# Kernel optimization log

Hardware: AMD Instinct MI355X
Metric: run time of the kernel (lower is better)

## Reference

```python
import jax, jax.numpy as jnp
import numpy as np

B, DIM_IN, T = 16, 512, 2048
DIM_OUT2 = 512 * 2  # dim_out * 2 (GLU halves it)
K = 3
STYLE = 128
SCALE_CONV = 1.0 / np.sqrt(DIM_IN * K ** 2).astype(np.float32)  # fan_in = dim_in * k^2 (as in source)
SCALE_LIN = 1.0 / np.sqrt(STYLE).astype(np.float32)


def setup_inputs() -> dict:
    key = jax.random.key(0)
    ks = jax.random.split(key, 6)
    x = jax.random.normal(ks[0], (B, DIM_IN, T), dtype=jnp.float32)
    c_src = jax.random.normal(ks[1], (B, STYLE), dtype=jnp.float32)
    c_trg = jax.random.normal(ks[2], (B, STYLE), dtype=jnp.float32)
    # EqualLinear params (lr_mul=1): weight ~ N(0,1), bias filled with bias_init=1
    w_s = jax.random.normal(ks[3], (DIM_IN, STYLE), dtype=jnp.float32)
    b_s = jnp.ones((DIM_IN,), dtype=jnp.float32)
    w_b = jax.random.normal(ks[4], (DIM_IN, STYLE), dtype=jnp.float32)
    b_b = jnp.ones((DIM_IN,), dtype=jnp.float32)
    weight = jax.random.normal(ks[5], (1, DIM_OUT2, DIM_IN, K), dtype=jnp.float32)
    return {"x": x, "c_src": c_src, "c_trg": c_trg,
            "w_s": w_s, "b_s": b_s, "w_b": w_b, "b_b": b_b, "weight": weight}


def reference(x, c_src, c_trg, w_s, b_s, w_b, b_b, weight):
    bsz, cin, t = x.shape
    cout = weight.shape[1]  # dim_out * 2
    k = weight.shape[3]
    # EqualLinear: F.linear(c, w*scale, bias)
    s = (c_trg @ (w_s * SCALE_LIN).T + b_s).reshape(bsz, 1, cin, 1)
    beta = (c_trg @ (w_b * SCALE_LIN).T + b_b).reshape(bsz, 1, cin, 1)
    w = SCALE_CONV * (weight * s + beta)               # [B, Cout, Cin, K]
    demod = jax.lax.rsqrt(jnp.sum(w * w, axis=(2, 3)) + 1e-8)   # [B, Cout]
    demod_mean = jnp.mean(w.reshape(bsz, cout, -1), axis=2)      # [B, Cout]
    w = (w - demod_mean[:, :, None, None]) * demod[:, :, None, None]
    # batch-as-groups conv1d
    w = w.reshape(bsz * cout, cin, k)
    xr = x.reshape(1, bsz * cin, t)
    out = jax.lax.conv_general_dilated(
        xr, w, window_strides=(1,), padding=[(k // 2, k // 2)],
        dimension_numbers=("NCH", "OIH", "NCH"), feature_group_count=bsz)
    out = out.reshape(bsz, cout, -1)
    a, g = jnp.split(out, 2, axis=1)  # GLU on channel dim
    return a * jax.nn.sigmoid(g)
```

## Files before the change

### kernel.cpp

```cpp
#include <hip/hip_runtime.h>
#include <math.h>

typedef __attribute__((ext_vector_type(8))) short short8;
typedef __attribute__((ext_vector_type(4))) float f32x4;
typedef unsigned short ushortT;

#define NB     16
#define CIN    512
#define TT     2048
#define COUT2  1024
#define NSTYLE 128
#define KKTOT  1536
#define TPAD   2050
#define NKT    24

#define SCALE_LIN  0.088388347648318447f
#define SCALE_CONV 0.014731391274719736f

__device__ __forceinline__ ushortT f2bf(float f) {
  union { float f; unsigned u; } v; v.f = f;
  unsigned r = v.u + 0x7fffu + ((v.u >> 16) & 1u);
  return (ushortT)(r >> 16);
}

__device__ __forceinline__ void gload16(const void* g, void* l) {
  __builtin_amdgcn_global_load_lds(
      (const __attribute__((address_space(1))) void*)g,
      (__attribute__((address_space(3))) void*)l, 16, 0, 0);
}

__global__ void style_kernel(const float* __restrict__ c_trg,
                             const float* __restrict__ w_s, const float* __restrict__ b_s,
                             const float* __restrict__ w_b, const float* __restrict__ b_b,
                             float* __restrict__ s, float* __restrict__ beta,
                             ushortT* __restrict__ xT) {
  int gid = blockIdx.x * 256 + threadIdx.x;
  int b = gid >> 9, ci = gid & 511;
  const float* ct = c_trg + b * NSTYLE;
  const float* ws = w_s + ci * NSTYLE;
  const float* wb = w_b + ci * NSTYLE;
  float as = 0.f, ab = 0.f;
#pragma unroll 8
  for (int j = 0; j < NSTYLE; ++j) {
    float c = ct[j];
    as += c * ws[j];
    ab += c * wb[j];
  }
  s[gid]    = as * SCALE_LIN + b_s[ci];
  beta[gid] = ab * SCALE_LIN + b_b[ci];
  xT[(size_t)b * TPAD * CIN + ci] = 0;
  xT[((size_t)b * TPAD + TPAD - 1) * CIN + ci] = 0;
}

__global__ void xpose_kernel(const float* __restrict__ x, ushortT* __restrict__ xT) {
  int b = blockIdx.z, ct = blockIdx.y, tt = blockIdx.x;
  int t0 = tt * 64, ci0 = ct * 64;
  __shared__ float tile[64][65];
  const float* xB = x + (size_t)b * CIN * TT;
  int rr = threadIdx.x >> 4;
  int c4 = threadIdx.x & 15;
#pragma unroll
  for (int it = 0; it < 4; ++it) {
    int ci = rr + it * 16;
    float4 v = *(const float4*)(xB + (size_t)(ci0 + ci) * TT + t0 + c4 * 4);
    tile[ci][c4 * 4 + 0] = v.x; tile[ci][c4 * 4 + 1] = v.y;
    tile[ci][c4 * 4 + 2] = v.z; tile[ci][c4 * 4 + 3] = v.w;
  }
  __syncthreads();
  ushortT* xTB = xT + (size_t)b * TPAD * CIN;
#pragma unroll
  for (int it = 0; it < 4; ++it) {
    int t = rr + it * 16;
    ushort4 o;
    o.x = f2bf(tile[c4 * 4 + 0][t]); o.y = f2bf(tile[c4 * 4 + 1][t]);
    o.z = f2bf(tile[c4 * 4 + 2][t]); o.w = f2bf(tile[c4 * 4 + 3][t]);
    *(ushort4*)(xTB + (size_t)(1 + t0 + t) * CIN + ci0 + c4 * 4) = o;
  }
}

__global__ void modw_kernel(const float* __restrict__ weight,
                            const float* __restrict__ s, const float* __restrict__ beta,
                            ushortT* __restrict__ wnorm) {
  int co = blockIdx.x, b = blockIdx.y, tid = threadIdx.x;
  int ci = tid * 2;
  const float* wp = weight + (size_t)co * CIN * 3 + (size_t)ci * 3;
  float s0 = s[b * CIN + ci],     s1 = s[b * CIN + ci + 1];
  float e0 = beta[b * CIN + ci],  e1 = beta[b * CIN + ci + 1];
  float w0 = SCALE_CONV * (wp[0] * s0 + e0);
  float w1 = SCALE_CONV * (wp[1] * s0 + e0);
  float w2 = SCALE_CONV * (wp[2] * s0 + e0);
  float w3 = SCALE_CONV * (wp[3] * s1 + e1);
  float w4 = SCALE_CONV * (wp[4] * s1 + e1);
  float w5 = SCALE_CONV * (wp[5] * s1 + e1);
  float sum = w0 + w1 + w2 + w3 + w4 + w5;
  float sq  = w0*w0 + w1*w1 + w2*w2 + w3*w3 + w4*w4 + w5*w5;
#pragma unroll
  for (int off = 32; off; off >>= 1) {
    sum += __shfl_xor(sum, off);
    sq  += __shfl_xor(sq,  off);
  }
  __shared__ float rs[4], rq[4];
  if ((tid & 63) == 0) { rs[tid >> 6] = sum; rq[tid >> 6] = sq; }
  __syncthreads();
  float tsum = rs[0] + rs[1] + rs[2] + rs[3];
  float tsq  = rq[0] + rq[1] + rq[2] + rq[3];
  float mean  = tsum * (1.0f / 1536.0f);
  float demod = rsqrtf(tsq + 1e-8f);
  int r = ((co & 511) << 1) | (co >> 9);
  ushortT* dst = wnorm + ((size_t)b * COUT2 + r) * KKTOT;
  ushort2 p0, p1, p2;
  p0.x = f2bf((w0 - mean) * demod); p0.y = f2bf((w3 - mean) * demod);
  p1.x = f2bf((w1 - mean) * demod); p1.y = f2bf((w4 - mean) * demod);
  p2.x = f2bf((w2 - mean) * demod); p2.y = f2bf((w5 - mean) * demod);
  *(ushort2*)(dst +        ci) = p0;
  *(ushort2*)(dst +  512 + ci) = p1;
  *(ushort2*)(dst + 1024 + ci) = p2;
}


#define AFRAG(d, s, f) (*(const short8*)(ldsc + ((d) * 4 + (s)) * 16384 + aoff + (f) * 1024))
#define BFRAG(d, s, g) (*(const short8*)(ldsc + ((d) * 4 + 2 + (s)) * 16384 + boff + (g) * 1024))

#define STAGE_A(d, s, kt) do {                                                   \
    int kc_ = (kt) * 64 + (s) * 32;                                              \
    gload16(wB + (size_t)(co0 + r0) * KKTOT + kc_ + jbs8,                        \
            ldsw + ((d) * 4 + (s)) * 8192 + tid * 8);                            \
    gload16(wB + (size_t)(co0 + r0 + 128) * KKTOT + kc_ + jbs8,                  \
            ldsw + ((d) * 4 + (s)) * 8192 + 4096 + tid * 8);                     \
  } while (0)

#define STAGE_B(d, s, kt) do {                                                   \
    int kc_ = (kt) * 64 + (s) * 32;                                              \
    int tap_ = kc_ >> 9; int ci_ = kc_ & 511;                                    \
    gload16(xB + (size_t)(t0 + r0 + tap_) * CIN + ci_ + jbs8,                    \
            ldsw + ((d) * 4 + 2 + (s)) * 8192 + tid * 8);                        \
    gload16(xB + (size_t)(t0 + r0 + 128 + tap_) * CIN + ci_ + jbs8,              \
            ldsw + ((d) * 4 + 2 + (s)) * 8192 + 4096 + tid * 8);                 \
  } while (0)

#define PHASE(d, s, mh, STAGES, VMN) do {                                        \
    short8 a0 = AFRAG(d, s, (mh) * 4 + 0);                                       \
    short8 a1 = AFRAG(d, s, (mh) * 4 + 1);                                       \
    short8 a2 = AFRAG(d, s, (mh) * 4 + 2);                                       \
    short8 a3 = AFRAG(d, s, (mh) * 4 + 3);                                       \
    if ((mh) == 0) {                                                             \
      bf0 = BFRAG(d, s, 0); bf1 = BFRAG(d, s, 1);                                \
      bf2 = BFRAG(d, s, 2); bf3 = BFRAG(d, s, 3);                                \
    }                                                                            \
    STAGES;                                                                      \
    if ((VMN) == 6)      asm volatile("s_waitcnt vmcnt(6)" ::: "memory");        \
    else if ((VMN) == 0) asm volatile("s_waitcnt vmcnt(0)" ::: "memory");        \
    __builtin_amdgcn_sched_barrier(0);                                           \
    __builtin_amdgcn_s_barrier();                                                \
    __builtin_amdgcn_sched_barrier(0);                                           \
    __builtin_amdgcn_s_setprio(1);                                               \
    acc[(mh)*4+0][0] = __builtin_amdgcn_mfma_f32_16x16x32_bf16(a0, bf0, acc[(mh)*4+0][0], 0, 0, 0); \
    acc[(mh)*4+0][1] = __builtin_amdgcn_mfma_f32_16x16x32_bf16(a0, bf1, acc[(mh)*4+0][1], 0, 0, 0); \
    acc[(mh)*4+0][2] = __builtin_amdgcn_mfma_f32_16x16x32_bf16(a0, bf2, acc[(mh)*4+0][2], 0, 0, 0); \
    acc[(mh)*4+0][3] = __builtin_amdgcn_mfma_f32_16x16x32_bf16(a0, bf3, acc[(mh)*4+0][3], 0, 0, 0); \
    acc[(mh)*4+1][0] = __builtin_amdgcn_mfma_f32_16x16x32_bf16(a1, bf0, acc[(mh)*4+1][0], 0, 0, 0); \
    acc[(mh)*4+1][1] = __builtin_amdgcn_mfma_f32_16x16x32_bf16(a1, bf1, acc[(mh)*4+1][1], 0, 0, 0); \
    acc[(mh)*4+1][2] = __builtin_amdgcn_mfma_f32_16x16x32_bf16(a1, bf2, acc[(mh)*4+1][2], 0, 0, 0); \
    acc[(mh)*4+1][3] = __builtin_amdgcn_mfma_f32_16x16x32_bf16(a1, bf3, acc[(mh)*4+1][3], 0, 0, 0); \
    acc[(mh)*4+2][0] = __builtin_amdgcn_mfma_f32_16x16x32_bf16(a2, bf0, acc[(mh)*4+2][0], 0, 0, 0); \
    acc[(mh)*4+2][1] = __builtin_amdgcn_mfma_f32_16x16x32_bf16(a2, bf1, acc[(mh)*4+2][1], 0, 0, 0); \
    acc[(mh)*4+2][2] = __builtin_amdgcn_mfma_f32_16x16x32_bf16(a2, bf2, acc[(mh)*4+2][2], 0, 0, 0); \
    acc[(mh)*4+2][3] = __builtin_amdgcn_mfma_f32_16x16x32_bf16(a2, bf3, acc[(mh)*4+2][3], 0, 0, 0); \
    acc[(mh)*4+3][0] = __builtin_amdgcn_mfma_f32_16x16x32_bf16(a3, bf0, acc[(mh)*4+3][0], 0, 0, 0); \
    acc[(mh)*4+3][1] = __builtin_amdgcn_mfma_f32_16x16x32_bf16(a3, bf1, acc[(mh)*4+3][1], 0, 0, 0); \
    acc[(mh)*4+3][2] = __builtin_amdgcn_mfma_f32_16x16x32_bf16(a3, bf2, acc[(mh)*4+3][2], 0, 0, 0); \
    acc[(mh)*4+3][3] = __builtin_amdgcn_mfma_f32_16x16x32_bf16(a3, bf3, acc[(mh)*4+3][3], 0, 0, 0); \
    __builtin_amdgcn_s_setprio(0);                                               \
    __builtin_amdgcn_sched_barrier(0);                                           \
    __builtin_amdgcn_s_barrier();                                                \
    __builtin_amdgcn_sched_barrier(0);                                           \
  } while (0)

__global__ __launch_bounds__(512, 2)
void conv_gemm8(const ushortT* __restrict__ wnorm, const ushortT* __restrict__ xT,
                float* __restrict__ out) {
  extern __shared__ ushortT ldsw[];
  const char* ldsc = (const char*)ldsw;

  int orig = blockIdx.x;
  int wgid = (orig & 7) * 64 + (orig >> 3);
  int b  = wgid >> 5;
  int i5 = wgid & 31;
  int mp = i5 >> 4, r2 = i5 & 15;
  int nt = r2 >> 1, mt = mp * 2 + (r2 & 1);
  int co0 = mt * 256, t0 = nt * 256;

  int tid = threadIdx.x;
  int l = tid & 63, w = tid >> 6;
  int wm = w & 1, wn = w >> 1;

  int r0 = tid >> 2;
  int jbs8 = (((tid & 3) ^ ((r0 >> 1) & 3)) << 3);
  int cb = ((l >> 4) ^ ((l >> 1) & 3));
  int aoff = (wm * 128 + (l & 15)) * 64 + cb * 16;
  int boff = (wn * 64  + (l & 15)) * 64 + cb * 16;

  const ushortT* wB = wnorm + (size_t)b * COUT2 * KKTOT;
  const ushortT* xB = xT + (size_t)b * TPAD * CIN;

  f32x4 acc[8][4];
#pragma unroll
  for (int i = 0; i < 8; ++i)
#pragma unroll
    for (int j = 0; j < 4; ++j)
      acc[i][j] = (f32x4){0.f, 0.f, 0.f, 0.f};
  short8 bf0 = {}, bf1 = {}, bf2 = {}, bf3 = {};

  STAGE_A(0, 0, 0); STAGE_B(0, 0, 0); STAGE_A(0, 1, 0); STAGE_B(0, 1, 0);
  STAGE_B(1, 0, 1); STAGE_A(1, 0, 1); STAGE_B(1, 1, 1);
  asm volatile("s_waitcnt vmcnt(6)" ::: "memory");
  __builtin_amdgcn_sched_barrier(0);
  __builtin_amdgcn_s_barrier();
  __builtin_amdgcn_sched_barrier(0);

  for (int j = 0; j < 11; ++j) {
    int kt1 = 2 * j + 1;
    int ktn0 = 2 * j + 2, ktn1 = 2 * j + 3;
    PHASE(0, 0, 0, STAGE_A(1, 1, kt1),  -1);
    PHASE(0, 0, 1, STAGE_B(0, 0, ktn0), -1);
    PHASE(0, 1, 0, STAGE_A(0, 0, ktn0), -1);
    PHASE(0, 1, 1, STAGE_B(0, 1, ktn0),  6);
    PHASE(1, 0, 0, STAGE_A(0, 1, ktn0), -1);
    PHASE(1, 0, 1, STAGE_B(1, 0, ktn1), -1);
    PHASE(1, 1, 0, STAGE_A(1, 0, ktn1), -1);
    PHASE(1, 1, 1, STAGE_B(1, 1, ktn1),  6);
  }
  PHASE(0, 0, 0, STAGE_A(1, 1, 23), -1);
  PHASE(0, 0, 1, {}, -1);
  PHASE(0, 1, 0, {}, -1);
  PHASE(0, 1, 1, {},  0);
  PHASE(1, 0, 0, {}, -1);
  PHASE(1, 0, 1, {}, -1);
  PHASE(1, 1, 0, {}, -1);
  PHASE(1, 1, 1, {}, -1);

#pragma unroll
  for (int f = 0; f < 8; ++f) {
    int cop = co0 + wm * 128 + f * 16 + ((l >> 4) << 2);
    int c = cop >> 1;
    size_t obase = ((size_t)b * (COUT2 / 2) + c) * TT;
#pragma unroll
    for (int g = 0; g < 4; ++g) {
      int t = t0 + wn * 64 + g * 16 + (l & 15);
      f32x4 v = acc[f][g];
      out[obase + t]      = v.x / (1.f + __expf(-v.y));
      out[obase + TT + t] = v.z / (1.f + __expf(-v.w));
    }
  }
}

extern "C" void kernel_launch(void* const* d_in, const int* in_sizes, int n_in,
                              void* d_out, int out_size, void* d_ws, size_t ws_size,
                              hipStream_t stream) {
  const float* x      = (const float*)d_in[0];
  const float* c_trg  = (const float*)d_in[2];
  const float* w_s    = (const float*)d_in[3];
  const float* b_s    = (const float*)d_in[4];
  const float* w_b    = (const float*)d_in[5];
  const float* b_b    = (const float*)d_in[6];
  const float* weight = (const float*)d_in[7];
  float* out = (float*)d_out;

  char* ws = (char*)d_ws;
  float*   s     = (float*)ws;
  float*   beta  = (float*)(ws + 32768);
  ushortT* xT    = (ushortT*)(ws + 65536);
  ushortT* wnorm = (ushortT*)(ws + 65536 + 33587200);

  hipFuncSetAttribute((const void*)conv_gemm8,
                      hipFuncAttributeMaxDynamicSharedMemorySize, 131072);

  style_kernel<<<32, 256, 0, stream>>>(c_trg, w_s, b_s, w_b, b_b, s, beta, xT);
  xpose_kernel<<<dim3(32, 8, 16), 256, 0, stream>>>(x, xT);
  modw_kernel<<<dim3(1024, 16), 256, 0, stream>>>(weight, s, beta, wnorm);
  conv_gemm8<<<512, 512, 131072, stream>>>(wnorm, xT, out);
}
```

Baseline: 136.8 us.

## Double-buffer LDS fragment registers to prefetch next phase during MFMA

Restructures the GEMM main loop so each phase issues LDS reads for the next phase's A/B fragments into alternate register sets before its MFMA block, overlapping LDS latency with matrix math. The vmcnt waits move to the end of phases with adjusted counts. This doubles fragment register usage (32 short8 vectors), which risks spills or occupancy pressure under launch_bounds(512,2), and it changes the correctness-critical sync ordering between global loads and LDS reads.

Result: no change. 136.4 us (-0.3%).

```diff
diff --git a/kernel.cpp b/kernel.cpp
--- a/kernel.cpp
+++ b/kernel.cpp
@@ -121,6 +121,20 @@
 #define AFRAG(d, s, f) (*(const short8*)(ldsc + ((d) * 4 + (s)) * 16384 + aoff + (f) * 1024))
 #define BFRAG(d, s, g) (*(const short8*)(ldsc + ((d) * 4 + 2 + (s)) * 16384 + boff + (g) * 1024))
 
+#define RDA(as_, d, s, mh) do {              \
+    as_##0 = AFRAG(d, s, (mh) * 4 + 0);      \
+    as_##1 = AFRAG(d, s, (mh) * 4 + 1);      \
+    as_##2 = AFRAG(d, s, (mh) * 4 + 2);      \
+    as_##3 = AFRAG(d, s, (mh) * 4 + 3);      \
+  } while (0)
+
+#define RDB(bs_, d, s) do {                  \
+    bs_##0 = BFRAG(d, s, 0);                 \
+    bs_##1 = BFRAG(d, s, 1);                 \
+    bs_##2 = BFRAG(d, s, 2);                 \
+    bs_##3 = BFRAG(d, s, 3);                 \
+  } while (0)
+
 #define STAGE_A(d, s, kt) do {                                                   \
     int kc_ = (kt) * 64 + (s) * 32;                                              \
     gload16(wB + (size_t)(co0 + r0) * KKTOT + kc_ + jbs8,                        \
@@ -138,40 +152,33 @@
             ldsw + ((d) * 4 + 2 + (s)) * 8192 + 4096 + tid * 8);                 \
   } while (0)
 
-#define PHASE(d, s, mh, STAGES, VMN) do {                                        \
-    short8 a0 = AFRAG(d, s, (mh) * 4 + 0);                                       \
-    short8 a1 = AFRAG(d, s, (mh) * 4 + 1);                                       \
-    short8 a2 = AFRAG(d, s, (mh) * 4 + 2);                                       \
-    short8 a3 = AFRAG(d, s, (mh) * 4 + 3);                                       \
-    if ((mh) == 0) {                                                             \
-      bf0 = BFRAG(d, s, 0); bf1 = BFRAG(d, s, 1);                                \
-      bf2 = BFRAG(d, s, 2); bf3 = BFRAG(d, s, 3);                                \
-    }                                                                            \
+#define PHASE(mh, au_, bu_, RD_CODE, STAGES, ENDVM) do {                         \
+    RD_CODE;                                                                     \
     STAGES;                                                                      \
-    if ((VMN) == 6)      asm volatile("s_waitcnt vmcnt(6)" ::: "memory");        \
-    else if ((VMN) == 0) asm volatile("s_waitcnt vmcnt(0)" ::: "memory");        \
     __builtin_amdgcn_sched_barrier(0);                                           \
     __builtin_amdgcn_s_barrier();                                                \
     __builtin_amdgcn_sched_barrier(0);                                           \
     __builtin_amdgcn_s_setprio(1);                                               \
-    acc[(mh)*4+0][0] = __builtin_amdgcn_mfma_f32_16x16x32_bf16(a0, bf0, acc[(mh)*4+0][0], 0, 0, 0); \
-    acc[(mh)*4+0][1] = __builtin_amdgcn_mfma_f32_16x16x32_bf16(a0, bf1, acc[(mh)*4+0][1], 0, 0, 0); \
-    acc[(mh)*4+0][2] = __builtin_amdgcn_mfma_f32_16x16x32_bf16(a0, bf2, acc[(mh)*4+0][2], 0, 0, 0); \
-    acc[(mh)*4+0][3] = __builtin_amdgcn_mfma_f32_16x16x32_bf16(a0, bf3, acc[(mh)*4+0][3], 0, 0, 0); \
-    acc[(mh)*4+1][0] = __builtin_amdgcn_mfma_f32_16x16x32_bf16(a1, bf0, acc[(mh)*4+1][0], 0, 0, 0); \
-    acc[(mh)*4+1][1] = __builtin_amdgcn_mfma_f32_16x16x32_bf16(a1, bf1, acc[(mh)*4+1][1], 0, 0, 0); \
-    acc[(mh)*4+1][2] = __builtin_amdgcn_mfma_f32_16x16x32_bf16(a1, bf2, acc[(mh)*4+1][2], 0, 0, 0); \
-    acc[(mh)*4+1][3] = __builtin_amdgcn_mfma_f32_16x16x32_bf16(a1, bf3, acc[(mh)*4+1][3], 0, 0, 0); \
-    acc[(mh)*4+2][0] = __builtin_amdgcn_mfma_f32_16x16x32_bf16(a2, bf0, acc[(mh)*4+2][0], 0, 0, 0); \
-    acc[(mh)*4+2][1] = __builtin_amdgcn_mfma_f32_16x16x32_bf16(a2, bf1, acc[(mh)*4+2][1], 0, 0, 0); \
-    acc[(mh)*4+2][2] = __builtin_amdgcn_mfma_f32_16x16x32_bf16(a2, bf2, acc[(mh)*4+2][2], 0, 0, 0); \
-    acc[(mh)*4+2][3] = __builtin_amdgcn_mfma_f32_16x16x32_bf16(a2, bf3, acc[(mh)*4+2][3], 0, 0, 0); \
-    acc[(mh)*4+3][0] = __builtin_amdgcn_mfma_f32_16x16x32_bf16(a3, bf0, acc[(mh)*4+3][0], 0, 0, 0); \
-    acc[(mh)*4+3][1] = __builtin_amdgcn_mfma_f32_16x16x32_bf16(a3, bf1, acc[(mh)*4+3][1], 0, 0, 0); \
-    acc[(mh)*4+3][2] = __builtin_amdgcn_mfma_f32_16x16x32_bf16(a3, bf2, acc[(mh)*4+3][2], 0, 0, 0); \
-    acc[(mh)*4+3][3] = __builtin_amdgcn_mfma_f32_16x16x32_bf16(a3, bf3, acc[(mh)*4+3][3], 0, 0, 0); \
+    acc[(mh)*4+0][0] = __builtin_amdgcn_mfma_f32_16x16x32_bf16(au_##0, bu_##0, acc[(mh)*4+0][0], 0, 0, 0); \
+    acc[(mh)*4+0][1] = __builtin_amdgcn_mfma_f32_16x16x32_bf16(au_##0, bu_##1, acc[(mh)*4+0][1], 0, 0, 0); \
+    acc[(mh)*4+0][2] = __builtin_amdgcn_mfma_f32_16x16x32_bf16(au_##0, bu_##2, acc[(mh)*4+0][2], 0, 0, 0); \
+    acc[(mh)*4+0][3] = __builtin_amdgcn_mfma_f32_16x16x32_bf16(au_##0, bu_##3, acc[(mh)*4+0][3], 0, 0, 0); \
+    acc[(mh)*4+1][0] = __builtin_amdgcn_mfma_f32_16x16x32_bf16(au_##1, bu_##0, acc[(mh)*4+1][0], 0, 0, 0); \
+    acc[(mh)*4+1][1] = __builtin_amdgcn_mfma_f32_16x16x32_bf16(au_##1, bu_##1, acc[(mh)*4+1][1], 0, 0, 0); \
+    acc[(mh)*4+1][2] = __builtin_amdgcn_mfma_f32_16x16x32_bf16(au_##1, bu_##2, acc[(mh)*4+1][2], 0, 0, 0); \
+    acc[(mh)*4+1][3] = __builtin_amdgcn_mfma_f32_16x16x32_bf16(au_##1, bu_##3, acc[(mh)*4+1][3], 0, 0, 0); \
+    acc[(mh)*4+2][0] = __builtin_amdgcn_mfma_f32_16x16x32_bf16(au_##2, bu_##0, acc[(mh)*4+2][0], 0, 0, 0); \
+    acc[(mh)*4+2][1] = __builtin_amdgcn_mfma_f32_16x16x32_bf16(au_##2, bu_##1, acc[(mh)*4+2][1], 0, 0, 0); \
+    acc[(mh)*4+2][2] = __builtin_amdgcn_mfma_f32_16x16x32_bf16(au_##2, bu_##2, acc[(mh)*4+2][2], 0, 0, 0); \
+    acc[(mh)*4+2][3] = __builtin_amdgcn_mfma_f32_16x16x32_bf16(au_##2, bu_##3, acc[(mh)*4+2][3], 0, 0, 0); \
+    acc[(mh)*4+3][0] = __builtin_amdgcn_mfma_f32_16x16x32_bf16(au_##3, bu_##0, acc[(mh)*4+3][0], 0, 0, 0); \
+    acc[(mh)*4+3][1] = __builtin_amdgcn_mfma_f32_16x16x32_bf16(au_##3, bu_##1, acc[(mh)*4+3][1], 0, 0, 0); \
+    acc[(mh)*4+3][2] = __builtin_amdgcn_mfma_f32_16x16x32_bf16(au_##3, bu_##2, acc[(mh)*4+3][2], 0, 0, 0); \
+    acc[(mh)*4+3][3] = __builtin_amdgcn_mfma_f32_16x16x32_bf16(au_##3, bu_##3, acc[(mh)*4+3][3], 0, 0, 0); \
     __builtin_amdgcn_s_setprio(0);                                               \
     __builtin_amdgcn_sched_barrier(0);                                           \
+    if ((ENDVM) == 8)      asm volatile("s_waitcnt vmcnt(8)" ::: "memory");      \
+    else if ((ENDVM) == 0) asm volatile("s_waitcnt vmcnt(0)" ::: "memory");      \
     __builtin_amdgcn_s_barrier();                                                \
     __builtin_amdgcn_sched_barrier(0);                                           \
   } while (0)
@@ -209,7 +216,10 @@
 #pragma unroll
     for (int j = 0; j < 4; ++j)
       acc[i][j] = (f32x4){0.f, 0.f, 0.f, 0.f};
-  short8 bf0 = {}, bf1 = {}, bf2 = {}, bf3 = {};
+  short8 ax0 = {}, ax1 = {}, ax2 = {}, ax3 = {};
+  short8 ay0 = {}, ay1 = {}, ay2 = {}, ay3 = {};
+  short8 bx0 = {}, bx1 = {}, bx2 = {}, bx3 = {};
+  short8 by0 = {}, by1 = {}, by2 = {}, by3 = {};
 
   STAGE_A(0, 0, 0); STAGE_B(0, 0, 0); STAGE_A(0, 1, 0); STAGE_B(0, 1, 0);
   STAGE_B(1, 0, 1); STAGE_A(1, 0, 1); STAGE_B(1, 1, 1);
@@ -217,27 +227,29 @@
   __builtin_amdgcn_sched_barrier(0);
   __builtin_amdgcn_s_barrier();
   __builtin_amdgcn_sched_barrier(0);
+  RDA(ax, 0, 0, 0);
+  RDB(bx, 0, 0);
 
   for (int j = 0; j < 11; ++j) {
     int kt1 = 2 * j + 1;
     int ktn0 = 2 * j + 2, ktn1 = 2 * j + 3;
-    PHASE(0, 0, 0, STAGE_A(1, 1, kt1),  -1);
-    PHASE(0, 0, 1, STAGE_B(0, 0, ktn0), -1);
-    PHASE(0, 1, 0, STAGE_A(0, 0, ktn0), -1);
-    PHASE(0, 1, 1, STAGE_B(0, 1, ktn0),  6);
-    PHASE(1, 0, 0, STAGE_A(0, 1, ktn0), -1);
-    PHASE(1, 0, 1, STAGE_B(1, 0, ktn1), -1);
-    PHASE(1, 1, 0, STAGE_A(1, 0, ktn1), -1);
-    PHASE(1, 1, 1, STAGE_B(1, 1, ktn1),  6);
-  }
-  PHASE(0, 0, 0, STAGE_A(1, 1, 23), -1);
-  PHASE(0, 0, 1, {}, -1);
-  PHASE(0, 1, 0, {}, -1);
-  PHASE(0, 1, 1, {},  0);
-  PHASE(1, 0, 0, {}, -1);
-  PHASE(1, 0, 1, {}, -1);
-  PHASE(1, 1, 0, {}, -1);
-  PHASE(1, 1, 1, {}, -1);
+    PHASE(0, ax, bx, { RDA(ay, 0, 0, 1); },                  STAGE_A(1, 1, kt1),   8);
+    PHASE(1, ay, bx, { RDA(ax, 0, 1, 0); RDB(by, 0, 1); },   STAGE_B(0, 0, ktn0), -1);
+    PHASE(0, ax, by, { RDA(ay, 0, 1, 1); },                  STAGE_A(0, 0, ktn0),  8);
+    PHASE(1, ay, by, { RDA(ax, 1, 0, 0); RDB(bx, 1, 0); },   STAGE_B(0, 1, ktn0), -1);
+    PHASE(0, ax, bx, { RDA(ay, 1, 0, 1); },                  STAGE_A(0, 1, ktn0),  8);
+    PHASE(1, ay, bx, { RDA(ax, 1, 1, 0); RDB(by, 1, 1); },   STAGE_B(1, 0, ktn1), -1);
+    PHASE(0, ax, by, { RDA(ay, 1, 1, 1); },                  STAGE_A(1, 0, ktn1),  8);
+    PHASE(1, ay, by, { RDA(ax, 0, 0, 0); RDB(bx, 0, 0); },   STAGE_B(1, 1, ktn1), -1);
+  }
+  PHASE(0, ax, bx, { RDA(ay, 0, 0, 1); },                  STAGE_A(1, 1, 23),     0);
+  PHASE(1, ay, bx, { RDA(ax, 0, 1, 0); RDB(by, 0, 1); },   {},                   -1);
+  PHASE(0, ax, by, { RDA(ay, 0, 1, 1); },                  {},                   -1);
+  PHASE(1, ay, by, { RDA(ax, 1, 0, 0); RDB(bx, 1, 0); },   {},                   -1);
+  PHASE(0, ax, bx, { RDA(ay, 1, 0, 1); },                  {},                   -1);
+  PHASE(1, ay, bx, { RDA(ax, 1, 1, 0); RDB(by, 1, 1); },   {},                   -1);
+  PHASE(0, ax, by, { RDA(ay, 1, 1, 1); },                  {},                   -1);
+  PHASE(1, ay, by, { },                                    {},                   -1);
 
 #pragma unroll
   for (int f = 0; f < 8; ++f) {
```

## Switch conv GEMM to 32x32x16 MFMA with restructured LDS fragment loads and pipeline

Applied to the files above, without the earlier changes.

Replaces the 16x16x32 bf16 MFMA tiling (8x4 accumulators per wave) with 32x32x16 MFMA (4x2 accumulators of 16 floats), changes the LDS fragment addressing and swizzle to match the 32-row layout, and merges the A/B staging so each phase issues both loads with a single wait count. This halves the number of phases and barriers per k-tile and reduces LDS fragment reads per MFMA FLOP. The GLU epilogue is rewritten for the new accumulator layout. It risks register pressure and changed store coalescing in the epilogue.

After: 148.8 us. 8.8% more time.

```diff
diff --git a/kernel.cpp b/kernel.cpp
--- a/kernel.cpp
+++ b/kernel.cpp
@@ -2,7 +2,7 @@
 #include <math.h>
 
 typedef __attribute__((ext_vector_type(8))) short short8;
-typedef __attribute__((ext_vector_type(4))) float f32x4;
+typedef __attribute__((ext_vector_type(16))) float f32x16;
 typedef unsigned short ushortT;
 
 #define NB     16
@@ -118,62 +118,44 @@
 }
 
 
-#define AFRAG(d, s, f) (*(const short8*)(ldsc + ((d) * 4 + (s)) * 16384 + aoff + (f) * 1024))
-#define BFRAG(d, s, g) (*(const short8*)(ldsc + ((d) * 4 + 2 + (s)) * 16384 + boff + (g) * 1024))
-
-#define STAGE_A(d, s, kt) do {                                                   \
-    int kc_ = (kt) * 64 + (s) * 32;                                              \
-    gload16(wB + (size_t)(co0 + r0) * KKTOT + kc_ + jbs8,                        \
-            ldsw + ((d) * 4 + (s)) * 8192 + tid * 8);                            \
-    gload16(wB + (size_t)(co0 + r0 + 128) * KKTOT + kc_ + jbs8,                  \
-            ldsw + ((d) * 4 + (s)) * 8192 + 4096 + tid * 8);                     \
+#define AF(d, s, m, k) (*(const short8*)(ldsc + ((d) * 4 + (s)) * 16384 + arow + (m) * 2048 + ((k) ? colk1 : colk0)))
+#define BF(d, s, n, k) (*(const short8*)(ldsc + ((d) * 4 + 2 + (s)) * 16384 + brow + (n) * 2048 + ((k) ? colk1 : colk0)))
+
+#define STAGE_A(d, s, kt) do { int kc_ = (kt) * 64 + (s) * 32;                  \
+    gload16(sA0 + kc_, ldsw + ((d) * 4 + (s)) * 8192 + dst8);                   \
+    gload16(sA1 + kc_, ldsw + ((d) * 4 + (s)) * 8192 + 4096 + dst8);            \
   } while (0)
 
-#define STAGE_B(d, s, kt) do {                                                   \
-    int kc_ = (kt) * 64 + (s) * 32;                                              \
-    int tap_ = kc_ >> 9; int ci_ = kc_ & 511;                                    \
-    gload16(xB + (size_t)(t0 + r0 + tap_) * CIN + ci_ + jbs8,                    \
-            ldsw + ((d) * 4 + 2 + (s)) * 8192 + tid * 8);                        \
-    gload16(xB + (size_t)(t0 + r0 + 128 + tap_) * CIN + ci_ + jbs8,              \
-            ldsw + ((d) * 4 + 2 + (s)) * 8192 + 4096 + tid * 8);                 \
+#define STAGE_B(d, s, kt) do { int kc_ = (kt) * 64 + (s) * 32;                  \
+    gload16(sB0 + kc_, ldsw + ((d) * 4 + 2 + (s)) * 8192 + dst8);               \
+    gload16(sB1 + kc_, ldsw + ((d) * 4 + 2 + (s)) * 8192 + 4096 + dst8);        \
   } while (0)
 
-#define PHASE(d, s, mh, STAGES, VMN) do {                                        \
-    short8 a0 = AFRAG(d, s, (mh) * 4 + 0);                                       \
-    short8 a1 = AFRAG(d, s, (mh) * 4 + 1);                                       \
-    short8 a2 = AFRAG(d, s, (mh) * 4 + 2);                                       \
-    short8 a3 = AFRAG(d, s, (mh) * 4 + 3);                                       \
-    if ((mh) == 0) {                                                             \
-      bf0 = BFRAG(d, s, 0); bf1 = BFRAG(d, s, 1);                                \
-      bf2 = BFRAG(d, s, 2); bf3 = BFRAG(d, s, 3);                                \
-    }                                                                            \
-    STAGES;                                                                      \
-    if ((VMN) == 6)      asm volatile("s_waitcnt vmcnt(6)" ::: "memory");        \
-    else if ((VMN) == 0) asm volatile("s_waitcnt vmcnt(0)" ::: "memory");        \
-    __builtin_amdgcn_sched_barrier(0);                                           \
-    __builtin_amdgcn_s_barrier();                                                \
-    __builtin_amdgcn_sched_barrier(0);                                           \
-    __builtin_amdgcn_s_setprio(1);                                               \
-    acc[(mh)*4+0][0] = __builtin_amdgcn_mfma_f32_16x16x32_bf16(a0, bf0, acc[(mh)*4+0][0], 0, 0, 0); \
-    acc[(mh)*4+0][1] = __builtin_amdgcn_mfma_f32_16x16x32_bf16(a0, bf1, acc[(mh)*4+0][1], 0, 0, 0); \
-    acc[(mh)*4+0][2] = __builtin_amdgcn_mfma_f32_16x16x32_bf16(a0, bf2, acc[(mh)*4+0][2], 0, 0, 0); \
-    acc[(mh)*4+0][3] = __builtin_amdgcn_mfma_f32_16x16x32_bf16(a0, bf3, acc[(mh)*4+0][3], 0, 0, 0); \
-    acc[(mh)*4+1][0] = __builtin_amdgcn_mfma_f32_16x16x32_bf16(a1, bf0, acc[(mh)*4+1][0], 0, 0, 0); \
-    acc[(mh)*4+1][1] = __builtin_amdgcn_mfma_f32_16x16x32_bf16(a1, bf1, acc[(mh)*4+1][1], 0, 0, 0); \
-    acc[(mh)*4+1][2] = __builtin_amdgcn_mfma_f32_16x16x32_bf16(a1, bf2, acc[(mh)*4+1][2], 0, 0, 0); \
-    acc[(mh)*4+1][3] = __builtin_amdgcn_mfma_f32_16x16x32_bf16(a1, bf3, acc[(mh)*4+1][3], 0, 0, 0); \
-    acc[(mh)*4+2][0] = __builtin_amdgcn_mfma_f32_16x16x32_bf16(a2, bf0, acc[(mh)*4+2][0], 0, 0, 0); \
-    acc[(mh)*4+2][1] = __builtin_amdgcn_mfma_f32_16x16x32_bf16(a2, bf1, acc[(mh)*4+2][1], 0, 0, 0); \
-    acc[(mh)*4+2][2] = __builtin_amdgcn_mfma_f32_16x16x32_bf16(a2, bf2, acc[(mh)*4+2][2], 0, 0, 0); \
-    acc[(mh)*4+2][3] = __builtin_amdgcn_mfma_f32_16x16x32_bf16(a2, bf3, acc[(mh)*4+2][3], 0, 0, 0); \
-    acc[(mh)*4+3][0] = __builtin_amdgcn_mfma_f32_16x16x32_bf16(a3, bf0, acc[(mh)*4+3][0], 0, 0, 0); \
-    acc[(mh)*4+3][1] = __builtin_amdgcn_mfma_f32_16x16x32_bf16(a3, bf1, acc[(mh)*4+3][1], 0, 0, 0); \
-    acc[(mh)*4+3][2] = __builtin_amdgcn_mfma_f32_16x16x32_bf16(a3, bf2, acc[(mh)*4+3][2], 0, 0, 0); \
-    acc[(mh)*4+3][3] = __builtin_amdgcn_mfma_f32_16x16x32_bf16(a3, bf3, acc[(mh)*4+3][3], 0, 0, 0); \
-    __builtin_amdgcn_s_setprio(0);                                               \
-    __builtin_amdgcn_sched_barrier(0);                                           \
-    __builtin_amdgcn_s_barrier();                                                \
-    __builtin_amdgcn_sched_barrier(0);                                           \
+#define PHASE(d, s, STAGES, VMN) do {                                           \
+    short8 af[4][2], bfr[2][2];                                                 \
+    _Pragma("unroll") for (int m_ = 0; m_ < 4; ++m_) {                          \
+      af[m_][0] = AF(d, s, m_, 0); af[m_][1] = AF(d, s, m_, 1);                 \
+    }                                                                           \
+    _Pragma("unroll") for (int n_ = 0; n_ < 2; ++n_) {                          \
+      bfr[n_][0] = BF(d, s, n_, 0); bfr[n_][1] = BF(d, s, n_, 1);               \
+    }                                                                           \
+    STAGES;                                                                     \
+    if ((VMN) == 8)      asm volatile("s_waitcnt vmcnt(8)" ::: "memory");       \
+    else if ((VMN) == 4) asm volatile("s_waitcnt vmcnt(4)" ::: "memory");       \
+    else if ((VMN) == 0) asm volatile("s_waitcnt vmcnt(0)" ::: "memory");       \
+    __builtin_amdgcn_sched_barrier(0);                                          \
+    __builtin_amdgcn_s_barrier();                                               \
+    __builtin_amdgcn_sched_barrier(0);                                          \
+    __builtin_amdgcn_s_setprio(1);                                              \
+    _Pragma("unroll") for (int k_ = 0; k_ < 2; ++k_)                            \
+      _Pragma("unroll") for (int m_ = 0; m_ < 4; ++m_)                          \
+        _Pragma("unroll") for (int n_ = 0; n_ < 2; ++n_)                        \
+          acc[m_][n_] = __builtin_amdgcn_mfma_f32_32x32x16_bf16(                \
+              af[m_][k_], bfr[n_][k_], acc[m_][n_], 0, 0, 0);                   \
+    __builtin_amdgcn_s_setprio(0);                                              \
+    __builtin_amdgcn_sched_barrier(0);                                          \
+    __builtin_amdgcn_s_barrier();                                               \
+    __builtin_amdgcn_sched_barrier(0);                                          \
   } while (0)
 
 __global__ __launch_bounds__(512, 2)
@@ -196,60 +178,58 @@
 
   int r0 = tid >> 2;
   int jbs8 = (((tid & 3) ^ ((r0 >> 1) & 3)) << 3);
-  int cb = ((l >> 4) ^ ((l >> 1) & 3));
-  int aoff = (wm * 128 + (l & 15)) * 64 + cb * 16;
-  int boff = (wn * 64  + (l & 15)) * 64 + cb * 16;
+  int dst8 = tid * 8;
+  int sw = (l >> 1) & 3;
+  int arow = (wm * 128 + (l & 31)) * 64;
+  int brow = (wn * 64  + (l & 31)) * 64;
+  int colk0 = (((l >> 5)    ) ^ sw) * 16;
+  int colk1 = (((l >> 5) | 2) ^ sw) * 16;
 
   const ushortT* wB = wnorm + (size_t)b * COUT2 * KKTOT;
   const ushortT* xB = xT + (size_t)b * TPAD * CIN;
-
-  f32x4 acc[8][4];
-#pragma unroll
-  for (int i = 0; i < 8; ++i)
-#pragma unroll
-    for (int j = 0; j < 4; ++j)
-      acc[i][j] = (f32x4){0.f, 0.f, 0.f, 0.f};
-  short8 bf0 = {}, bf1 = {}, bf2 = {}, bf3 = {};
-
-  STAGE_A(0, 0, 0); STAGE_B(0, 0, 0); STAGE_A(0, 1, 0); STAGE_B(0, 1, 0);
-  STAGE_B(1, 0, 1); STAGE_A(1, 0, 1); STAGE_B(1, 1, 1);
-  asm volatile("s_waitcnt vmcnt(6)" ::: "memory");
+  const ushortT* sA0 = wB + (size_t)(co0 + r0) * KKTOT + jbs8;
+  const ushortT* sA1 = sA0 + (size_t)128 * KKTOT;
+  const ushortT* sB0 = xB + (size_t)(t0 + r0) * CIN + jbs8;
+  const ushortT* sB1 = sB0 + (size_t)128 * CIN;
+
+  f32x16 acc[4][2] = {};
+
+  STAGE_A(0, 0, 0); STAGE_B(0, 0, 0);
+  STAGE_A(0, 1, 0); STAGE_B(0, 1, 0);
+  STAGE_A(1, 0, 1); STAGE_B(1, 0, 1);
+  asm volatile("s_waitcnt vmcnt(8)" ::: "memory");
   __builtin_amdgcn_sched_barrier(0);
   __builtin_amdgcn_s_barrier();
   __builtin_amdgcn_sched_barrier(0);
 
   for (int j = 0; j < 11; ++j) {
     int kt1 = 2 * j + 1;
-    int ktn0 = 2 * j + 2, ktn1 = 2 * j + 3;
-    PHASE(0, 0, 0, STAGE_A(1, 1, kt1),  -1);
-    PHASE(0, 0, 1, STAGE_B(0, 0, ktn0), -1);
-    PHASE(0, 1, 0, STAGE_A(0, 0, ktn0), -1);
-    PHASE(0, 1, 1, STAGE_B(0, 1, ktn0),  6);
-    PHASE(1, 0, 0, STAGE_A(0, 1, ktn0), -1);
-    PHASE(1, 0, 1, STAGE_B(1, 0, ktn1), -1);
-    PHASE(1, 1, 0, STAGE_A(1, 0, ktn1), -1);
-    PHASE(1, 1, 1, STAGE_B(1, 1, ktn1),  6);
-  }
-  PHASE(0, 0, 0, STAGE_A(1, 1, 23), -1);
-  PHASE(0, 0, 1, {}, -1);
-  PHASE(0, 1, 0, {}, -1);
-  PHASE(0, 1, 1, {},  0);
-  PHASE(1, 0, 0, {}, -1);
-  PHASE(1, 0, 1, {}, -1);
-  PHASE(1, 1, 0, {}, -1);
-  PHASE(1, 1, 1, {}, -1);
-
-#pragma unroll
-  for (int f = 0; f < 8; ++f) {
-    int cop = co0 + wm * 128 + f * 16 + ((l >> 4) << 2);
-    int c = cop >> 1;
-    size_t obase = ((size_t)b * (COUT2 / 2) + c) * TT;
-#pragma unroll
-    for (int g = 0; g < 4; ++g) {
-      int t = t0 + wn * 64 + g * 16 + (l & 15);
-      f32x4 v = acc[f][g];
-      out[obase + t]      = v.x / (1.f + __expf(-v.y));
-      out[obase + TT + t] = v.z / (1.f + __expf(-v.w));
+    int k0n = 2 * j + 2, k1n = 2 * j + 3;
+    PHASE(0, 0, { STAGE_A(1, 1, kt1); STAGE_B(1, 1, kt1); }, 8);
+    PHASE(0, 1, { STAGE_A(0, 0, k0n); STAGE_B(0, 0, k0n); }, 8);
+    PHASE(1, 0, { STAGE_A(0, 1, k0n); STAGE_B(0, 1, k0n); }, 8);
+    PHASE(1, 1, { STAGE_A(1, 0, k1n); STAGE_B(1, 0, k1n); }, 8);
+  }
+  PHASE(0, 0, { STAGE_A(1, 1, 23); STAGE_B(1, 1, 23); }, 8);
+  PHASE(0, 1, {}, 4);
+  PHASE(1, 0, {}, 0);
+  PHASE(1, 1, {}, -1);
+
+  int hi4 = (l >> 5) * 4;
+#pragma unroll
+  for (int m = 0; m < 4; ++m) {
+    int cobase = co0 + wm * 128 + m * 32;
+#pragma unroll
+    for (int n = 0; n < 2; ++n) {
+      int t = t0 + wn * 64 + n * 32 + (l & 31);
+      f32x16 v = acc[m][n];
+#pragma unroll
+      for (int q = 0; q < 8; ++q) {
+        int row = 2 * (q & 1) + 8 * (q >> 1) + hi4;
+        int c = (cobase + row) >> 1;
+        float a = v[2 * q], g = v[2 * q + 1];
+        out[((size_t)b * (COUT2 / 2) + c) * TT + t] = a / (1.f + __expf(-g));
+      }
     }
   }
 }
```
